# Performance work log

Measured on AMD Instinct MI355X. Metric: run time of the kernel, lower is better.

## Reference

```python
import jax, jax.numpy as jnp
import numpy as np

B, T, H, W = 8, 16, 512, 512


def setup_inputs() -> dict:
    key = jax.random.key(0)
    k1, k2 = jax.random.split(key)
    img = jax.random.normal(k1, (B, H, W), dtype=jnp.float32)
    U = jax.random.normal(k2, (B, T, H, W, 2), dtype=jnp.float32)
    return {"img": img, "U": U}


def _warp(img, U):
    # img: (B,H,W), U: (B,T,H,W,2) displacement (di, dj). Output (B,T,H,W).
    b, h, w = img.shape
    ii = jnp.arange(h, dtype=jnp.float32)[:, None]   # (H,1)
    jj = jnp.arange(w, dtype=jnp.float32)[None, :]   # (1,W)
    si = ii - U[..., 0]                              # (B,T,H,W) sample rows
    sj = jj - U[..., 1]                              # (B,T,H,W) sample cols
    i0 = jnp.clip(jnp.floor(si).astype(jnp.int32), 0, h - 1)
    j0 = jnp.clip(jnp.floor(sj).astype(jnp.int32), 0, w - 1)
    i1 = jnp.clip(i0 + 1, 0, h - 1)
    j1 = jnp.clip(j0 + 1, 0, w - 1)
    # fractional weights computed AFTER clipping, matching the original
    di = si - i0.astype(jnp.float32)
    dj = sj - j0.astype(jnp.float32)

    def gather(im, ri, ci):  # im (H,W), ri/ci (T,H,W)
        return im[ri, ci]

    g = jax.vmap(gather)  # over batch
    f00 = g(img, i0, j0)
    f01 = g(img, i0, j1)
    f10 = g(img, i1, j0)
    f11 = g(img, i1, j1)
    f0 = f00 + (f01 - f00) * dj
    f1 = f10 + (f11 - f10) * dj
    return f0 + (f1 - f0) * di


def reference(img, U):
    return _warp(img, U)
```

## Files before the change

### kernel.cpp

```cpp
#include <hip/hip_runtime.h>

#define HH 512
#define WW 512
#define TT 16
#define ROWS 2
#define NR 13
#define OFF 5

typedef float vf4 __attribute__((ext_vector_type(4)));
typedef float vf2 __attribute__((ext_vector_type(2)));

__device__ __forceinline__ float warp_one(const float* __restrict__ lds,
                                          const float* __restrict__ im,
                                          int ip, float fi, float fj,
                                          float ux, float uy) {
    float si = fi - ux;
    float sj = fj - uy;
    int i0 = (int)floorf(si);
    int j0 = (int)floorf(sj);
    i0 = min(max(i0, 0), HH - 1);
    j0 = min(max(j0, 0), WW - 1);
    int i1 = min(i0 + 1, HH - 1);
    int j1 = min(j0 + 1, WW - 1);
    float di = si - (float)i0;
    float dj = sj - (float)j0;
    int s0 = i0 - ip + OFF;
    int s1 = i1 - ip + OFF;
    float f00, f01, f10, f11;
    if (((unsigned)s0 < NR) & ((unsigned)s1 < NR)) {
        f00 = lds[s0 * WW + j0];
        f01 = lds[s0 * WW + j1];
        f10 = lds[s1 * WW + j0];
        f11 = lds[s1 * WW + j1];
    } else {
        f00 = im[i0 * WW + j0];
        f01 = im[i0 * WW + j1];
        f10 = im[i1 * WW + j0];
        f11 = im[i1 * WW + j1];
    }
    float f0 = f00 + (f01 - f00) * dj;
    float f1 = f10 + (f11 - f10) * dj;
    return f0 + (f1 - f0) * di;
}

__global__ __launch_bounds__(256) void SpatialWarp_kernel(
    const float* __restrict__ img,
    const float* __restrict__ U,
    float* __restrict__ out)
{
    __shared__ float lds[NR * WW];

    int bid = blockIdx.x;
    int b  = bid >> 8;
    int ip = (bid & 255) << 1;
    const float* im = img + (size_t)b * (HH * WW);

    int k = threadIdx.x;
    int j = k << 1;
    float fj0 = (float)j, fj1 = (float)(j + 1);
    float fi0 = (float)ip, fi1 = (float)(ip + 1);

    size_t ubase = (((size_t)b * TT) * HH + ip) * (WW / 2);
    const vf4* Uv = reinterpret_cast<const vf4*>(U);

    vf4 u0c = __builtin_nontemporal_load(Uv + ubase + k);
    vf4 u1c = __builtin_nontemporal_load(Uv + ubase + (WW / 2) + k);

    for (int idx = threadIdx.x; idx < NR * (WW / 4); idx += 256) {
        int s = idx >> 7;
        int c = idx & 127;
        int r = min(max(ip - OFF + s, 0), HH - 1);
        reinterpret_cast<vf4*>(lds)[idx] =
            reinterpret_cast<const vf4*>(im + (size_t)r * WW)[c];
    }
    __syncthreads();

    size_t ostride = (size_t)HH * WW;
#pragma unroll
    for (int t = 0; t < TT; ++t) {
        vf4 u0n, u1n;
        if (t < TT - 1) {
            size_t un = ubase + (size_t)(t + 1) * HH * (WW / 2);
            u0n = __builtin_nontemporal_load(Uv + un + k);
            u1n = __builtin_nontemporal_load(Uv + un + (WW / 2) + k);
        }
        float r00 = warp_one(lds, im, ip, fi0, fj0, u0c.x, u0c.y);
        float r01 = warp_one(lds, im, ip, fi0, fj1, u0c.z, u0c.w);
        float r10 = warp_one(lds, im, ip, fi1, fj0, u1c.x, u1c.y);
        float r11 = warp_one(lds, im, ip, fi1, fj1, u1c.z, u1c.w);

        size_t obase = (((size_t)b * TT + t) * HH + ip) * WW;
        vf2 rv0; rv0.x = r00; rv0.y = r01;
        vf2 rv1; rv1.x = r10; rv1.y = r11;
        __builtin_nontemporal_store(rv0, reinterpret_cast<vf2*>(out + obase) + k);
        __builtin_nontemporal_store(rv1, reinterpret_cast<vf2*>(out + obase + WW) + k);

        u0c = u0n; u1c = u1n;
    }
    (void)ostride;
}

extern "C" void kernel_launch(void* const* d_in, const int* in_sizes, int n_in,
                              void* d_out, int out_size, void* d_ws, size_t ws_size,
                              hipStream_t stream) {
    const float* img = (const float*)d_in[0];
    const float* U   = (const float*)d_in[1];
    float* out = (float*)d_out;

    dim3 block(256);
    dim3 grid(8 * (HH / ROWS));
    hipLaunchKernelGGL(SpatialWarp_kernel, grid, block, 0, stream,
                       img, U, out);
}
```

Baseline: 82.41 us.

## Remap threads to one row by four columns, shrink LDS halo, pair loads

Each thread now handles four consecutive pixels in a single row instead of a 2x2 patch, so U is read as two contiguous float4s and output is written as one float4 store. The LDS row halo is reduced from 13 to 11 rows, which cuts the staging load and shared memory use. Horizontal neighbor reads in LDS now use adjacent addresses with an edge select instead of computing a clamped j1. A smaller halo sends more samples to the global-memory fallback path when displacements are large.

```diff
diff --git a/kernel.cpp b/kernel.cpp
--- a/kernel.cpp
+++ b/kernel.cpp
@@ -3,14 +3,12 @@
 #define HH 512
 #define WW 512
 #define TT 16
-#define ROWS 2
-#define NR 13
-#define OFF 5
+#define NR 11
+#define OFF 4
 
 typedef float vf4 __attribute__((ext_vector_type(4)));
-typedef float vf2 __attribute__((ext_vector_type(2)));
 
-__device__ __forceinline__ float warp_one(const float* __restrict__ lds,
+__device__ __forceinline__ float warp_one(const float* __restrict__ lds_,
                                           const float* __restrict__ im,
                                           int ip, float fi, float fj,
                                           float ux, float uy) {
@@ -21,18 +19,21 @@
     i0 = min(max(i0, 0), HH - 1);
     j0 = min(max(j0, 0), WW - 1);
     int i1 = min(i0 + 1, HH - 1);
-    int j1 = min(j0 + 1, WW - 1);
     float di = si - (float)i0;
     float dj = sj - (float)j0;
     int s0 = i0 - ip + OFF;
     int s1 = i1 - ip + OFF;
     float f00, f01, f10, f11;
     if (((unsigned)s0 < NR) & ((unsigned)s1 < NR)) {
-        f00 = lds[s0 * WW + j0];
-        f01 = lds[s0 * WW + j1];
-        f10 = lds[s1 * WW + j0];
-        f11 = lds[s1 * WW + j1];
+        const float* p0 = lds_ + s0 * WW + j0;
+        const float* p1 = lds_ + s1 * WW + j0;
+        float a0 = p0[0], b0 = p0[1];
+        float a1 = p1[0], b1 = p1[1];
+        bool edge = (j0 == WW - 1);
+        f00 = a0; f01 = edge ? a0 : b0;
+        f10 = a1; f11 = edge ? a1 : b1;
     } else {
+        int j1 = min(j0 + 1, WW - 1);
         f00 = im[i0 * WW + j0];
         f01 = im[i0 * WW + j1];
         f10 = im[i1 * WW + j0];
@@ -48,56 +49,56 @@
     const float* __restrict__ U,
     float* __restrict__ out)
 {
-    __shared__ float lds[NR * WW];
+    __shared__ __align__(16) float lds[NR * WW + 4];
 
     int bid = blockIdx.x;
     int b  = bid >> 8;
     int ip = (bid & 255) << 1;
     const float* im = img + (size_t)b * (HH * WW);
 
-    int k = threadIdx.x;
-    int j = k << 1;
+    int r = threadIdx.x >> 7;
+    int q = threadIdx.x & 127;
+    int j = q << 2;
+    int irow = ip + r;
+    float fi  = (float)irow;
     float fj0 = (float)j, fj1 = (float)(j + 1);
-    float fi0 = (float)ip, fi1 = (float)(ip + 1);
+    float fj2 = (float)(j + 2), fj3 = (float)(j + 3);
 
-    size_t ubase = (((size_t)b * TT) * HH + ip) * (WW / 2);
     const vf4* Uv = reinterpret_cast<const vf4*>(U);
+    size_t uidx  = (((size_t)b * TT) * HH + irow) * (WW / 2) + ((size_t)q << 1);
+    size_t ustep = (size_t)HH * (WW / 2);
 
-    vf4 u0c = __builtin_nontemporal_load(Uv + ubase + k);
-    vf4 u1c = __builtin_nontemporal_load(Uv + ubase + (WW / 2) + k);
+    vf4 ua = __builtin_nontemporal_load(Uv + uidx);
+    vf4 ub = __builtin_nontemporal_load(Uv + uidx + 1);
 
     for (int idx = threadIdx.x; idx < NR * (WW / 4); idx += 256) {
         int s = idx >> 7;
         int c = idx & 127;
-        int r = min(max(ip - OFF + s, 0), HH - 1);
+        int rr = min(max(ip - OFF + s, 0), HH - 1);
         reinterpret_cast<vf4*>(lds)[idx] =
-            reinterpret_cast<const vf4*>(im + (size_t)r * WW)[c];
+            reinterpret_cast<const vf4*>(im + (size_t)rr * WW)[c];
     }
     __syncthreads();
 
-    size_t ostride = (size_t)HH * WW;
 #pragma unroll
     for (int t = 0; t < TT; ++t) {
-        vf4 u0n, u1n;
+        vf4 na, nb;
         if (t < TT - 1) {
-            size_t un = ubase + (size_t)(t + 1) * HH * (WW / 2);
-            u0n = __builtin_nontemporal_load(Uv + un + k);
-            u1n = __builtin_nontemporal_load(Uv + un + (WW / 2) + k);
+            size_t un = uidx + (size_t)(t + 1) * ustep;
+            na = __builtin_nontemporal_load(Uv + un);
+            nb = __builtin_nontemporal_load(Uv + un + 1);
         }
-        float r00 = warp_one(lds, im, ip, fi0, fj0, u0c.x, u0c.y);
-        float r01 = warp_one(lds, im, ip, fi0, fj1, u0c.z, u0c.w);
-        float r10 = warp_one(lds, im, ip, fi1, fj0, u1c.x, u1c.y);
-        float r11 = warp_one(lds, im, ip, fi1, fj1, u1c.z, u1c.w);
+        float r0 = warp_one(lds, im, ip, fi, fj0, ua.x, ua.y);
+        float r1 = warp_one(lds, im, ip, fi, fj1, ua.z, ua.w);
+        float r2 = warp_one(lds, im, ip, fi, fj2, ub.x, ub.y);
+        float r3 = warp_one(lds, im, ip, fi, fj3, ub.z, ub.w);
 
-        size_t obase = (((size_t)b * TT + t) * HH + ip) * WW;
-        vf2 rv0; rv0.x = r00; rv0.y = r01;
-        vf2 rv1; rv1.x = r10; rv1.y = r11;
-        __builtin_nontemporal_store(rv0, reinterpret_cast<vf2*>(out + obase) + k);
-        __builtin_nontemporal_store(rv1, reinterpret_cast<vf2*>(out + obase + WW) + k);
+        vf4 rv; rv.x = r0; rv.y = r1; rv.z = r2; rv.w = r3;
+        size_t oidx = (((size_t)b * TT + t) * HH + irow) * (WW / 4) + q;
+        __builtin_nontemporal_store(rv, reinterpret_cast<vf4*>(out) + oidx);
 
-        u0c = u0n; u1c = u1n;
+        ua = na; ub = nb;
     }
-    (void)ostride;
 }
 
 extern "C" void kernel_launch(void* const* d_in, const int* in_sizes, int n_in,
@@ -108,7 +109,7 @@
     float* out = (float*)d_out;
 
     dim3 block(256);
-    dim3 grid(8 * (HH / ROWS));
+    dim3 grid(8 * (HH / 2));
     hipLaunchKernelGGL(SpatialWarp_kernel, grid, block, 0, stream,
                        img, U, out);
 }
```

Measured after the change: 87.92 us. 1.07x slower.
